# Kernel tuning notes

Measured on AMD Instinct MI355X. Metric: run time of the kernel, lower is better.

The kernel has to match this reference:

```python
import jax, jax.numpy as jnp
import numpy as np

# dims
B, QL, KL = 2, 1024, 4096
HID = 2048            # hidden_size
H, HD, RD = 16, 128, 64   # heads, head_dim, rope_dim
G = 4                 # gla_num_groups
HPG = H // G          # heads_per_group
QLR = 512             # q low-rank (W_dQ out)
LAT = 256             # latent_dim_per_group
KVP = G * LAT         # kv_proj_dim
EPS = 1e-6


def rmsnorm(x, w):
    var = jnp.mean(jnp.square(x.astype(jnp.float32)), axis=-1, keepdims=True)
    return (x * jax.lax.rsqrt(var + EPS)).astype(x.dtype) * w


def setup_inputs() -> dict:
    key = jax.random.key(0)
    ks = jax.random.split(key, 8)
    s = 0.02
    return {
        "x_q": jax.random.normal(ks[0], (B, QL, HID), jnp.float32),
        "x_kv": jax.random.normal(ks[1], (B, KL, HID), jnp.float32),
        "W_dQ": jax.random.normal(ks[2], (HID, QLR), jnp.float32) * s,
        "q_norm_w": jnp.ones((QLR,), jnp.float32),
        "W_uQ": jax.random.normal(ks[3], (QLR, H * (HD + RD)), jnp.float32) * s,
        "W_dKV": jax.random.normal(ks[4], (HID, KVP + RD), jnp.float32) * s,
        "kv_norm_w": jnp.ones((G, LAT), jnp.float32),
        "W_ukv": jax.random.normal(ks[5], (G, LAT, HPG * 2 * HD), jnp.float32) * s,
        "W_o": jax.random.normal(ks[6], (H * HD, HID), jnp.float32) * s,
    }


def reference(x_q, x_kv, W_dQ, q_norm_w, W_uQ, W_dKV, kv_norm_w, W_ukv, W_o):
    b, ql, _ = x_q.shape
    kl = x_kv.shape[1]
    # --- query path: down-proj -> RMSNorm -> up-proj -> drop rope dims ---
    q = rmsnorm(x_q @ W_dQ, q_norm_w)                       # [b, ql, QLR]
    q = (q @ W_uQ).reshape(b, ql, H, HD + RD)[..., :HD]     # [b, ql, H, HD]
    # --- kv path: down-proj -> slice -> per-group RMSNorm -> grouped up-proj ---
    ckv = (x_kv @ W_dKV)[..., :KVP].reshape(b, kl, G, LAT)  # [b, kl, G, LAT]
    ckv = rmsnorm(ckv, kv_norm_w)                           # weight [G, LAT] broadcasts
    kv = jnp.einsum("bsgl,gld->bsgd", ckv, W_ukv)           # [b, kl, G, HPG*2*HD]
    kv = kv.reshape(b, kl, H, 2 * HD)                       # group-major head order
    k, v = kv[..., :HD], kv[..., HD:]
    # --- SDPA (no mask, non-causal) ---
    scale = 1.0 / np.sqrt(HD).astype(np.float32)
    scores = jnp.einsum("bqhd,bkhd->bhqk", q, k) * scale    # [b, H, ql, kl]
    p = jax.nn.softmax(scores, axis=-1)
    out = jnp.einsum("bhqk,bkhd->bqhd", p, v).reshape(b, ql, H * HD)
    return out @ W_o
```

## Files before the change

kernel.cpp:

```cpp
#include <hip/hip_runtime.h>
#include <hip/hip_bf16.h>
#include <math.h>


typedef __attribute__((ext_vector_type(8))) short short8;
typedef __attribute__((ext_vector_type(4))) float f32x4;

__device__ __forceinline__ ushort f2bf(float x) {
    __hip_bfloat16 h = __float2bfloat16(x);
    return *reinterpret_cast<ushort*>(&h);
}

__global__ __launch_bounds__(256) void cast_bf16(const float* __restrict__ src,
        ushort* __restrict__ dst)
{
    size_t i = ((size_t)blockIdx.x * 256 + threadIdx.x) * 8;
    float4 a = *(const float4*)(src + i);
    float4 b = *(const float4*)(src + i + 4);
    ushort u[8] = {f2bf(a.x), f2bf(a.y), f2bf(a.z), f2bf(a.w),
                   f2bf(b.x), f2bf(b.y), f2bf(b.z), f2bf(b.w)};
    *(uint4*)(dst + i) = *(uint4*)u;
}

__global__ __launch_bounds__(256) void transpose_cast(const float* __restrict__ src,
        ushort* __restrict__ dst, int srl, int dstld, int remap,
        long src_z, long dst_z)
{
    __shared__ ushort tile[64][68];
    const int k0 = blockIdx.x * 64;
    const int n0 = blockIdx.y * 64;
    src += (size_t)blockIdx.z * src_z;
    dst += (size_t)blockIdx.z * dst_z;
    const int cb = n0 + (remap ? (n0 >> 7) * 64 : 0);
    const int t = threadIdx.x;
    {
        int r = t >> 4, c4 = t & 15;
        #pragma unroll
        for (int i = 0; i < 4; ++i) {
            float4 v = *(const float4*)(src + (size_t)(k0 + r + 16 * i) * srl + cb + c4 * 4);
            tile[r + 16 * i][c4 * 4 + 0] = f2bf(v.x);
            tile[r + 16 * i][c4 * 4 + 1] = f2bf(v.y);
            tile[r + 16 * i][c4 * 4 + 2] = f2bf(v.z);
            tile[r + 16 * i][c4 * 4 + 3] = f2bf(v.w);
        }
    }
    __syncthreads();
    {
        int n = t >> 4, k4 = t & 15;
        #pragma unroll
        for (int i = 0; i < 4; ++i) {
            ushort4 v;
            v.x = tile[k4 * 4 + 0][n + 16 * i];
            v.y = tile[k4 * 4 + 1][n + 16 * i];
            v.z = tile[k4 * 4 + 2][n + 16 * i];
            v.w = tile[k4 * 4 + 3][n + 16 * i];
            *(ushort4*)(dst + (size_t)(n0 + n + 16 * i) * dstld + k0 + k4 * 4) = v;
        }
    }
}

__global__ __launch_bounds__(256) void gemm_mfma(const ushort* __restrict__ A,
        const ushort* __restrict__ Bt, void* __restrict__ Cv,
        int M, int N, int K, int lda, int ldb, int ldc, int obf16, float scale)
{
    __shared__ ushort As[128][72];
    __shared__ ushort Bs[128][72];
    const int tid = threadIdx.x;
    const int w = tid >> 6, lane = tid & 63;
    const int quad = lane >> 4, l16 = lane & 15;
    const int wm = (w >> 1) * 64, wn = (w & 1) * 64;
    const int m0 = blockIdx.y * 128, n0 = blockIdx.x * 128;

    f32x4 acc[4][4];
    #pragma unroll
    for (int i = 0; i < 4; ++i)
        #pragma unroll
        for (int j = 0; j < 4; ++j) acc[i][j] = (f32x4){0.f, 0.f, 0.f, 0.f};

    const int str = tid >> 3;
    const int stc = (tid & 7) * 8;

    for (int k0 = 0; k0 < K; k0 += 64) {
        __syncthreads();
        #pragma unroll
        for (int i = 0; i < 4; ++i) {
            int r = str + 32 * i;
            *(uint4*)&As[r][stc] = *(const uint4*)(A + (size_t)(m0 + r) * lda + k0 + stc);
            *(uint4*)&Bs[r][stc] = *(const uint4*)(Bt + (size_t)(n0 + r) * ldb + k0 + stc);
        }
        __syncthreads();
        #pragma unroll
        for (int kc = 0; kc < 2; ++kc) {
            short8 af[4], bf[4];
            #pragma unroll
            for (int i = 0; i < 4; ++i) {
                af[i] = *(const short8*)&As[wm + i * 16 + l16][kc * 32 + quad * 8];
                bf[i] = *(const short8*)&Bs[wn + i * 16 + l16][kc * 32 + quad * 8];
            }
            #pragma unroll
            for (int i = 0; i < 4; ++i)
                #pragma unroll
                for (int j = 0; j < 4; ++j)
                    acc[i][j] = __builtin_amdgcn_mfma_f32_16x16x32_bf16(af[i], bf[j], acc[i][j], 0, 0, 0);
        }
    }
    if (!obf16) {
        float* C = (float*)Cv;
        #pragma unroll
        for (int i = 0; i < 4; ++i)
            #pragma unroll
            for (int r = 0; r < 4; ++r) {
                float* cp = C + (size_t)(m0 + wm + i * 16 + quad * 4 + r) * ldc + n0 + wn + l16;
                #pragma unroll
                for (int j = 0; j < 4; ++j) cp[j * 16] = acc[i][j][r] * scale;
            }
    } else {
        ushort* C = (ushort*)Cv;
        #pragma unroll
        for (int i = 0; i < 4; ++i)
            #pragma unroll
            for (int r = 0; r < 4; ++r) {
                ushort* cp = C + (size_t)(m0 + wm + i * 16 + quad * 4 + r) * ldc + n0 + wn + l16;
                #pragma unroll
                for (int j = 0; j < 4; ++j) cp[j * 16] = f2bf(acc[i][j][r] * scale);
            }
    }
}

__global__ __launch_bounds__(256) void rms_q_wave(const float* __restrict__ x,
        const float* __restrict__ w, ushort* __restrict__ dst)
{
    const int row = blockIdx.x * 4 + (threadIdx.x >> 6);
    const int lane = threadIdx.x & 63;
    const float* p = x + (size_t)row * 512;
    float4 v0 = *(const float4*)(p + lane * 4);
    float4 v1 = *(const float4*)(p + 256 + lane * 4);
    float ss = v0.x*v0.x + v0.y*v0.y + v0.z*v0.z + v0.w*v0.w
             + v1.x*v1.x + v1.y*v1.y + v1.z*v1.z + v1.w*v1.w;
    #pragma unroll
    for (int m = 1; m < 64; m <<= 1) ss += __shfl_xor(ss, m);
    float inv = rsqrtf(ss * (1.f / 512.f) + 1e-6f);
    float4 w0 = *(const float4*)(w + lane * 4);
    float4 w1 = *(const float4*)(w + 256 + lane * 4);
    ushort* dp = dst + (size_t)row * 512;
    ushort4 o0, o1;
    o0.x = f2bf(v0.x * inv * w0.x); o0.y = f2bf(v0.y * inv * w0.y);
    o0.z = f2bf(v0.z * inv * w0.z); o0.w = f2bf(v0.w * inv * w0.w);
    o1.x = f2bf(v1.x * inv * w1.x); o1.y = f2bf(v1.y * inv * w1.y);
    o1.z = f2bf(v1.z * inv * w1.z); o1.w = f2bf(v1.w * inv * w1.w);
    *(ushort4*)(dp + lane * 4)       = o0;
    *(ushort4*)(dp + 256 + lane * 4) = o1;
}

__global__ __launch_bounds__(256) void rms_kv_wave(const float* __restrict__ x,
        const float* __restrict__ w, ushort* __restrict__ dst)
{
    const int idx = blockIdx.x * 4 + (threadIdx.x >> 6);
    const int lane = threadIdx.x & 63;
    const int r = idx >> 2, g = idx & 3;
    const float* p = x + (size_t)r * 1024 + g * 256;
    float4 v = *(const float4*)(p + lane * 4);
    float ss = v.x*v.x + v.y*v.y + v.z*v.z + v.w*v.w;
    #pragma unroll
    for (int m = 1; m < 64; m <<= 1) ss += __shfl_xor(ss, m);
    float inv = rsqrtf(ss * (1.f / 256.f) + 1e-6f);
    float4 wv = *(const float4*)(w + g * 256 + lane * 4);
    ushort4 o;
    o.x = f2bf(v.x * inv * wv.x); o.y = f2bf(v.y * inv * wv.y);
    o.z = f2bf(v.z * inv * wv.z); o.w = f2bf(v.w * inv * wv.w);
    *(ushort4*)(dst + (size_t)r * 1024 + g * 256 + lane * 4) = o;
}

__global__ __launch_bounds__(256) void transpose_v(const ushort* __restrict__ KVb,
                                                   ushort* __restrict__ Vt)
{
    __shared__ ushort tile[64][66];
    const int s0 = blockIdx.x * 64;
    const int d0 = blockIdx.y * 64;
    const int bh = blockIdx.z;
    const int b = bh >> 4, h = bh & 15, g = h >> 2, p = h & 3;
    const int t = threadIdx.x;
    const ushort* src = KVb + (size_t)g * 8388608ull + (size_t)(b * 4096) * 1024 + p * 256 + 128;
    {
        int sl = t >> 4, c4 = t & 15;
        #pragma unroll
        for (int i = 0; i < 4; ++i) {
            int s = sl + 16 * i;
            ushort4 v = *(const ushort4*)(src + (size_t)(s0 + s) * 1024 + d0 + c4 * 4);
            tile[s][c4 * 4 + 0] = v.x; tile[s][c4 * 4 + 1] = v.y;
            tile[s][c4 * 4 + 2] = v.z; tile[s][c4 * 4 + 3] = v.w;
        }
    }
    __syncthreads();
    {
        int dl = t >> 4, s4 = t & 15;
        ushort* dst = Vt + (size_t)(b * 16 + h) * 128 * 4096;
        #pragma unroll
        for (int i = 0; i < 4; ++i) {
            int d = dl + 16 * i;
            ushort4 v;
            v.x = tile[s4 * 4 + 0][d]; v.y = tile[s4 * 4 + 1][d];
            v.z = tile[s4 * 4 + 2][d]; v.w = tile[s4 * 4 + 3][d];
            *(ushort4*)(dst + (size_t)(d0 + d) * 4096 + s0 + s4 * 4) = v;
        }
    }
}

__global__ __launch_bounds__(256) void attn_mfma_split(const ushort* __restrict__ Qb,
        const ushort* __restrict__ KVb, const ushort* __restrict__ Vt,
        float* __restrict__ Opart, float* __restrict__ ml)
{
    __shared__ ushort Ks[64][136];
    __shared__ ushort VsT[128][72];
    __shared__ ushort Ps[4][16][72];

    const int q0 = blockIdx.x * 64;
    const int h = blockIdx.y;
    const int b = blockIdx.z >> 1, chunk = blockIdx.z & 1;
    const int g = h >> 2, p = h & 3;
    const int tid = threadIdx.x;
    const int w = tid >> 6, lane = tid & 63;
    const int quad = lane >> 4, l16 = lane & 15;
    const int sbase = chunk * 2048;

    const ushort* qg = Qb + (size_t)(b * 1024 + q0) * 2048 + h * 128;
    const ushort* kg = KVb + (size_t)g * 8388608ull + (size_t)(b * 4096 + sbase) * 1024 + p * 256;
    const ushort* vg = Vt + (size_t)(b * 16 + h) * 128 * 4096 + sbase;

    {
        int r = tid >> 4, c8 = tid & 15;
        #pragma unroll
        for (int i = 0; i < 4; ++i)
            *(uint4*)&Ks[r + 16 * i][c8 * 8] =
                *(const uint4*)(qg + (size_t)(r + 16 * i) * 2048 + c8 * 8);
    }
    __syncthreads();
    short8 qf[4];
    {
        int qr = w * 16 + l16;
        #pragma unroll
        for (int kc = 0; kc < 4; ++kc)
            qf[kc] = *(const short8*)&Ks[qr][kc * 32 + quad * 8];
    }

    f32x4 accO[8];
    float m_i[4], l_i[4];
    #pragma unroll
    for (int dt = 0; dt < 8; ++dt) accO[dt] = (f32x4){0.f, 0.f, 0.f, 0.f};
    #pragma unroll
    for (int r = 0; r < 4; ++r) { m_i[r] = -INFINITY; l_i[r] = 0.f; }

    for (int s0 = 0; s0 < 2048; s0 += 64) {
        __syncthreads();
        {
            int r = tid >> 4, c8 = tid & 15;
            #pragma unroll
            for (int i = 0; i < 4; ++i)
                *(uint4*)&Ks[r + 16 * i][c8 * 8] =
                    *(const uint4*)(kg + (size_t)(s0 + r + 16 * i) * 1024 + c8 * 8);
            int d = tid >> 3, s8 = tid & 7;
            #pragma unroll
            for (int i = 0; i < 4; ++i)
                *(uint4*)&VsT[d + 32 * i][s8 * 8] =
                    *(const uint4*)(vg + (size_t)(d + 32 * i) * 4096 + s0 + s8 * 8);
        }
        __syncthreads();
        f32x4 accS[4];
        #pragma unroll
        for (int st = 0; st < 4; ++st) accS[st] = (f32x4){0.f, 0.f, 0.f, 0.f};
        #pragma unroll
        for (int kc = 0; kc < 4; ++kc) {
            #pragma unroll
            for (int st = 0; st < 4; ++st) {
                short8 kf = *(const short8*)&Ks[st * 16 + l16][kc * 32 + quad * 8];
                accS[st] = __builtin_amdgcn_mfma_f32_16x16x32_bf16(qf[kc], kf, accS[st], 0, 0, 0);
            }
        }
        #pragma unroll
        for (int r = 0; r < 4; ++r) {
            float tm = fmaxf(fmaxf(accS[0][r], accS[1][r]), fmaxf(accS[2][r], accS[3][r]));
            #pragma unroll
            for (int msk = 1; msk < 16; msk <<= 1) tm = fmaxf(tm, __shfl_xor(tm, msk));
            float mn = fmaxf(m_i[r], tm);
            float alpha = __expf(m_i[r] - mn);
            float rs = 0.f;
            #pragma unroll
            for (int st = 0; st < 4; ++st) {
                float e = __expf(accS[st][r] - mn);
                rs += e;
                Ps[w][quad * 4 + r][st * 16 + l16] = f2bf(e);
            }
            #pragma unroll
            for (int msk = 1; msk < 16; msk <<= 1) rs += __shfl_xor(rs, msk);
            l_i[r] = l_i[r] * alpha + rs;
            m_i[r] = mn;
            #pragma unroll
            for (int dt = 0; dt < 8; ++dt) accO[dt][r] *= alpha;
        }
        __syncthreads();
        short8 pf[2];
        #pragma unroll
        for (int sc = 0; sc < 2; ++sc)
            pf[sc] = *(const short8*)&Ps[w][l16][sc * 32 + quad * 8];
        #pragma unroll
        for (int sc = 0; sc < 2; ++sc) {
            #pragma unroll
            for (int dt = 0; dt < 8; ++dt) {
                short8 vf = *(const short8*)&VsT[dt * 16 + l16][sc * 32 + quad * 8];
                accO[dt] = __builtin_amdgcn_mfma_f32_16x16x32_bf16(pf[sc], vf, accO[dt], 0, 0, 0);
            }
        }
    }
    const int qrow = q0 + w * 16 + quad * 4;
    float* ob = Opart + (size_t)((chunk * 2 + b) * 1024 + qrow) * 2048 + h * 128 + l16;
    #pragma unroll
    for (int r = 0; r < 4; ++r)
        #pragma unroll
        for (int dt = 0; dt < 8; ++dt)
            ob[(size_t)r * 2048 + dt * 16] = accO[dt][r];
    if (l16 == 0) {
        #pragma unroll
        for (int r = 0; r < 4; ++r) {
            size_t mi = ((size_t)((chunk * 2 + b) * 1024 + qrow + r) * 16 + h) * 2;
            ml[mi] = m_i[r];
            ml[mi + 1] = l_i[r];
        }
    }
}

__global__ __launch_bounds__(256) void attn_merge(const float* __restrict__ Opart,
        const float* __restrict__ ml, ushort* __restrict__ Om)
{
    const int idx = blockIdx.x * 4 + (threadIdx.x >> 6);
    const int lane = threadIdx.x & 63;
    const int h = idx & 15;
    const int q = (idx >> 4) & 1023;
    const int b = idx >> 14;

    size_t m1i = ((size_t)((0 * 2 + b) * 1024 + q) * 16 + h) * 2;
    size_t m2i = ((size_t)((1 * 2 + b) * 1024 + q) * 16 + h) * 2;
    float m1 = ml[m1i], l1 = ml[m1i + 1];
    float m2 = ml[m2i], l2 = ml[m2i + 1];
    float M = fmaxf(m1, m2);
    float w1 = __expf(m1 - M), w2 = __expf(m2 - M);
    float invL = 1.f / (l1 * w1 + l2 * w2);

    const float* o1 = Opart + (size_t)((0 * 2 + b) * 1024 + q) * 2048 + h * 128;
    const float* o2 = Opart + (size_t)((1 * 2 + b) * 1024 + q) * 2048 + h * 128;
    ushort* ob = Om + (size_t)(b * 1024 + q) * 2048 + h * 128;
    ob[lane]      = f2bf((o1[lane]      * w1 + o2[lane]      * w2) * invL);
    ob[lane + 64] = f2bf((o1[lane + 64] * w1 + o2[lane + 64] * w2) * invL);
}

extern "C" void kernel_launch(void* const* d_in, const int* in_sizes, int n_in,
                              void* d_out, int out_size, void* d_ws, size_t ws_size,
                              hipStream_t stream)
{
    (void)in_sizes; (void)n_in; (void)out_size; (void)ws_size;
    const float* x_q       = (const float*)d_in[0];
    const float* x_kv      = (const float*)d_in[1];
    const float* W_dQ      = (const float*)d_in[2];
    const float* q_norm_w  = (const float*)d_in[3];
    const float* W_uQ      = (const float*)d_in[4];
    const float* W_dKV     = (const float*)d_in[5];
    const float* kv_norm_w = (const float*)d_in[6];
    const float* W_ukv     = (const float*)d_in[7];
    const float* W_o       = (const float*)d_in[8];
    float* out = (float*)d_out;

    float* ws = (float*)d_ws;
    ushort* xkvb       = (ushort*)ws;
    ushort* attn_out_b = (ushort*)ws;
    float*  mlbuf      = ws + 2097152ull;
    ushort* Wot        = (ushort*)(ws + 4194304ull);
    float*  ckv        = ws + 8388608ull;
    float*  Opart      = ws + 8388608ull;
    ushort* xqb        = (ushort*)(ws + 8388608ull);
    ushort* WdQt       = (ushort*)(ws + 10485760ull);
    float*  q_lat      = ws + 11010048ull;
    ushort* q_lat_b    = (ushort*)(ws + 12058624ull);
    ushort* WuQt       = (ushort*)(ws + 12582912ull);
    ushort* ckv_b      = (ushort*)(ws + 16777216ull);
    ushort* kvgb       = (ushort*)(ws + 20971520ull);
    ushort* vt         = (ushort*)(ws + 37748736ull);
    ushort* qb         = (ushort*)(ws + 46137344ull);
    ushort* WdKVt      = (ushort*)(ws + 48234496ull);
    ushort* Wukvt      = (ushort*)(ws + 49283072ull);

    const float qscale = 0.08838834764831845f;

    cast_bf16<<<2048, 256, 0, stream>>>(x_q, xqb);
    transpose_cast<<<dim3(32, 8, 1), 256, 0, stream>>>(W_dQ, WdQt, 512, 2048, 0, 0, 0);
    gemm_mfma<<<dim3(4, 16), 256, 0, stream>>>(xqb, WdQt, q_lat, 2048, 512, 2048, 2048, 2048, 512, 0, 1.f);
    rms_q_wave<<<512, 256, 0, stream>>>(q_lat, q_norm_w, q_lat_b);
    transpose_cast<<<dim3(8, 32, 1), 256, 0, stream>>>(W_uQ, WuQt, 3072, 512, 1, 0, 0);
    gemm_mfma<<<dim3(16, 16), 256, 0, stream>>>(q_lat_b, WuQt, qb, 2048, 2048, 512, 512, 512, 2048, 1, qscale);
    cast_bf16<<<8192, 256, 0, stream>>>(x_kv, xkvb);
    transpose_cast<<<dim3(32, 16, 1), 256, 0, stream>>>(W_dKV, WdKVt, 1088, 2048, 0, 0, 0);
    gemm_mfma<<<dim3(8, 64), 256, 0, stream>>>(xkvb, WdKVt, ckv, 8192, 1024, 2048, 2048, 2048, 1024, 0, 1.f);
    rms_kv_wave<<<8192, 256, 0, stream>>>(ckv, kv_norm_w, ckv_b);
    transpose_cast<<<dim3(4, 16, 4), 256, 0, stream>>>(W_ukv, Wukvt, 1024, 256, 0, 262144, 262144);
    for (int g = 0; g < 4; ++g)
        gemm_mfma<<<dim3(8, 64), 256, 0, stream>>>(ckv_b + g * 256, Wukvt + (size_t)g * 262144,
                                                   kvgb + (size_t)g * 8388608ull,
                                                   8192, 1024, 256, 1024, 256, 1024, 1, 1.f);
    transpose_v<<<dim3(64, 2, 32), 256, 0, stream>>>(kvgb, vt);
    attn_mfma_split<<<dim3(16, 16, 4), 256, 0, stream>>>(qb, kvgb, vt, Opart, mlbuf);
    attn_merge<<<8192, 256, 0, stream>>>(Opart, mlbuf, attn_out_b);
    transpose_cast<<<dim3(32, 32, 1), 256, 0, stream>>>(W_o, Wot, 2048, 2048, 0, 0, 0);
    gemm_mfma<<<dim3(16, 16), 256, 0, stream>>>(attn_out_b, Wot, out, 2048, 2048, 2048, 2048, 2048, 2048, 0, 1.f);
}
```

Before: 555.5 us.

## Double per-wave query rows in attention and batch grouped KV up-projection GEMMs

The attention kernel now handles 128 query rows per block, 32 per wave as two 16-row tiles, so each K and V tile loaded into shared memory feeds twice as many MFMAs. Query fragments now come straight from global memory instead of being staged through shared memory. The four per-group KV up-projection GEMM launches become one launch using blockIdx.z with batch strides. In exchange the attention grid is halved to 512 blocks and register pressure grows from the doubled accumulators, which may reduce occupancy.

Measured after the change: 580.7 us. +4.5%, slower.

```diff
diff --git a/kernel.cpp b/kernel.cpp
--- a/kernel.cpp
+++ b/kernel.cpp
@@ -61,7 +61,8 @@
 
 __global__ __launch_bounds__(256) void gemm_mfma(const ushort* __restrict__ A,
         const ushort* __restrict__ Bt, void* __restrict__ Cv,
-        int M, int N, int K, int lda, int ldb, int ldc, int obf16, float scale)
+        int M, int N, int K, int lda, int ldb, int ldc, int obf16, float scale,
+        long strA, long strB, long strC)
 {
     __shared__ ushort As[128][72];
     __shared__ ushort Bs[128][72];
@@ -70,6 +71,8 @@
     const int quad = lane >> 4, l16 = lane & 15;
     const int wm = (w >> 1) * 64, wn = (w & 1) * 64;
     const int m0 = blockIdx.y * 128, n0 = blockIdx.x * 128;
+    A  += (size_t)blockIdx.z * strA;
+    Bt += (size_t)blockIdx.z * strB;
 
     f32x4 acc[4][4];
     #pragma unroll
@@ -105,7 +108,7 @@
         }
     }
     if (!obf16) {
-        float* C = (float*)Cv;
+        float* C = (float*)Cv + (size_t)blockIdx.z * strC;
         #pragma unroll
         for (int i = 0; i < 4; ++i)
             #pragma unroll
@@ -115,7 +118,7 @@
                 for (int j = 0; j < 4; ++j) cp[j * 16] = acc[i][j][r] * scale;
             }
     } else {
-        ushort* C = (ushort*)Cv;
+        ushort* C = (ushort*)Cv + (size_t)blockIdx.z * strC;
         #pragma unroll
         for (int i = 0; i < 4; ++i)
             #pragma unroll
@@ -212,9 +215,9 @@
 {
     __shared__ ushort Ks[64][136];
     __shared__ ushort VsT[128][72];
-    __shared__ ushort Ps[4][16][72];
-
-    const int q0 = blockIdx.x * 64;
+    __shared__ ushort Ps[4][32][72];
+
+    const int q0 = blockIdx.x * 128;
     const int h = blockIdx.y;
     const int b = blockIdx.z >> 1, chunk = blockIdx.z & 1;
     const int g = h >> 2, p = h & 3;
@@ -227,28 +230,23 @@
     const ushort* kg = KVb + (size_t)g * 8388608ull + (size_t)(b * 4096 + sbase) * 1024 + p * 256;
     const ushort* vg = Vt + (size_t)(b * 16 + h) * 128 * 4096 + sbase;
 
-    {
-        int r = tid >> 4, c8 = tid & 15;
-        #pragma unroll
-        for (int i = 0; i < 4; ++i)
-            *(uint4*)&Ks[r + 16 * i][c8 * 8] =
-                *(const uint4*)(qg + (size_t)(r + 16 * i) * 2048 + c8 * 8);
-    }
-    __syncthreads();
-    short8 qf[4];
-    {
-        int qr = w * 16 + l16;
+    short8 qf[2][4];
+    #pragma unroll
+    for (int qt = 0; qt < 2; ++qt)
         #pragma unroll
         for (int kc = 0; kc < 4; ++kc)
-            qf[kc] = *(const short8*)&Ks[qr][kc * 32 + quad * 8];
-    }
-
-    f32x4 accO[8];
-    float m_i[4], l_i[4];
-    #pragma unroll
-    for (int dt = 0; dt < 8; ++dt) accO[dt] = (f32x4){0.f, 0.f, 0.f, 0.f};
-    #pragma unroll
-    for (int r = 0; r < 4; ++r) { m_i[r] = -INFINITY; l_i[r] = 0.f; }
+            qf[qt][kc] = *(const short8*)(qg + (size_t)(w * 32 + qt * 16 + l16) * 2048
+                                          + kc * 32 + quad * 8);
+
+    f32x4 accO[2][8];
+    float m_i[2][4], l_i[2][4];
+    #pragma unroll
+    for (int qt = 0; qt < 2; ++qt) {
+        #pragma unroll
+        for (int dt = 0; dt < 8; ++dt) accO[qt][dt] = (f32x4){0.f, 0.f, 0.f, 0.f};
+        #pragma unroll
+        for (int r = 0; r < 4; ++r) { m_i[qt][r] = -INFINITY; l_i[qt][r] = 0.f; }
+    }
 
     for (int s0 = 0; s0 < 2048; s0 += 64) {
         __syncthreads();
@@ -265,65 +263,79 @@
                     *(const uint4*)(vg + (size_t)(d + 32 * i) * 4096 + s0 + s8 * 8);
         }
         __syncthreads();
-        f32x4 accS[4];
-        #pragma unroll
-        for (int st = 0; st < 4; ++st) accS[st] = (f32x4){0.f, 0.f, 0.f, 0.f};
+        f32x4 accS[2][4];
+        #pragma unroll
+        for (int qt = 0; qt < 2; ++qt)
+            #pragma unroll
+            for (int st = 0; st < 4; ++st) accS[qt][st] = (f32x4){0.f, 0.f, 0.f, 0.f};
         #pragma unroll
         for (int kc = 0; kc < 4; ++kc) {
-            #pragma unroll
-            for (int st = 0; st < 4; ++st) {
-                short8 kf = *(const short8*)&Ks[st * 16 + l16][kc * 32 + quad * 8];
-                accS[st] = __builtin_amdgcn_mfma_f32_16x16x32_bf16(qf[kc], kf, accS[st], 0, 0, 0);
-            }
-        }
-        #pragma unroll
-        for (int r = 0; r < 4; ++r) {
-            float tm = fmaxf(fmaxf(accS[0][r], accS[1][r]), fmaxf(accS[2][r], accS[3][r]));
-            #pragma unroll
-            for (int msk = 1; msk < 16; msk <<= 1) tm = fmaxf(tm, __shfl_xor(tm, msk));
-            float mn = fmaxf(m_i[r], tm);
-            float alpha = __expf(m_i[r] - mn);
-            float rs = 0.f;
-            #pragma unroll
-            for (int st = 0; st < 4; ++st) {
-                float e = __expf(accS[st][r] - mn);
-                rs += e;
-                Ps[w][quad * 4 + r][st * 16 + l16] = f2bf(e);
-            }
-            #pragma unroll
-            for (int msk = 1; msk < 16; msk <<= 1) rs += __shfl_xor(rs, msk);
-            l_i[r] = l_i[r] * alpha + rs;
-            m_i[r] = mn;
-            #pragma unroll
-            for (int dt = 0; dt < 8; ++dt) accO[dt][r] *= alpha;
-        }
+            short8 kf[4];
+            #pragma unroll
+            for (int st = 0; st < 4; ++st)
+                kf[st] = *(const short8*)&Ks[st * 16 + l16][kc * 32 + quad * 8];
+            #pragma unroll
+            for (int qt = 0; qt < 2; ++qt)
+                #pragma unroll
+                for (int st = 0; st < 4; ++st)
+                    accS[qt][st] = __builtin_amdgcn_mfma_f32_16x16x32_bf16(qf[qt][kc], kf[st], accS[qt][st], 0, 0, 0);
+        }
+        #pragma unroll
+        for (int qt = 0; qt < 2; ++qt)
+            #pragma unroll
+            for (int r = 0; r < 4; ++r) {
+                float tm = fmaxf(fmaxf(accS[qt][0][r], accS[qt][1][r]),
+                                 fmaxf(accS[qt][2][r], accS[qt][3][r]));
+                #pragma unroll
+                for (int msk = 1; msk < 16; msk <<= 1) tm = fmaxf(tm, __shfl_xor(tm, msk));
+                float mn = fmaxf(m_i[qt][r], tm);
+                float alpha = __expf(m_i[qt][r] - mn);
+                float rs = 0.f;
+                #pragma unroll
+                for (int st = 0; st < 4; ++st) {
+                    float e = __expf(accS[qt][st][r] - mn);
+                    rs += e;
+                    Ps[w][qt * 16 + quad * 4 + r][st * 16 + l16] = f2bf(e);
+                }
+                #pragma unroll
+                for (int msk = 1; msk < 16; msk <<= 1) rs += __shfl_xor(rs, msk);
+                l_i[qt][r] = l_i[qt][r] * alpha + rs;
+                m_i[qt][r] = mn;
+                #pragma unroll
+                for (int dt = 0; dt < 8; ++dt) accO[qt][dt][r] *= alpha;
+            }
         __syncthreads();
-        short8 pf[2];
-        #pragma unroll
-        for (int sc = 0; sc < 2; ++sc)
-            pf[sc] = *(const short8*)&Ps[w][l16][sc * 32 + quad * 8];
         #pragma unroll
         for (int sc = 0; sc < 2; ++sc) {
+            short8 pf[2];
+            #pragma unroll
+            for (int qt = 0; qt < 2; ++qt)
+                pf[qt] = *(const short8*)&Ps[w][qt * 16 + l16][sc * 32 + quad * 8];
             #pragma unroll
             for (int dt = 0; dt < 8; ++dt) {
                 short8 vf = *(const short8*)&VsT[dt * 16 + l16][sc * 32 + quad * 8];
-                accO[dt] = __builtin_amdgcn_mfma_f32_16x16x32_bf16(pf[sc], vf, accO[dt], 0, 0, 0);
-            }
-        }
-    }
-    const int qrow = q0 + w * 16 + quad * 4;
-    float* ob = Opart + (size_t)((chunk * 2 + b) * 1024 + qrow) * 2048 + h * 128 + l16;
-    #pragma unroll
-    for (int r = 0; r < 4; ++r)
-        #pragma unroll
-        for (int dt = 0; dt < 8; ++dt)
-            ob[(size_t)r * 2048 + dt * 16] = accO[dt][r];
-    if (l16 == 0) {
-        #pragma unroll
-        for (int r = 0; r < 4; ++r) {
-            size_t mi = ((size_t)((chunk * 2 + b) * 1024 + qrow + r) * 16 + h) * 2;
-            ml[mi] = m_i[r];
-            ml[mi + 1] = l_i[r];
+                #pragma unroll
+                for (int qt = 0; qt < 2; ++qt)
+                    accO[qt][dt] = __builtin_amdgcn_mfma_f32_16x16x32_bf16(pf[qt], vf, accO[qt][dt], 0, 0, 0);
+            }
+        }
+    }
+    #pragma unroll
+    for (int qt = 0; qt < 2; ++qt) {
+        const int qrow = q0 + w * 32 + qt * 16 + quad * 4;
+        float* ob = Opart + (size_t)((chunk * 2 + b) * 1024 + qrow) * 2048 + h * 128 + l16;
+        #pragma unroll
+        for (int r = 0; r < 4; ++r)
+            #pragma unroll
+            for (int dt = 0; dt < 8; ++dt)
+                ob[(size_t)r * 2048 + dt * 16] = accO[qt][dt][r];
+        if (l16 == 0) {
+            #pragma unroll
+            for (int r = 0; r < 4; ++r) {
+                size_t mi = ((size_t)((chunk * 2 + b) * 1024 + qrow + r) * 16 + h) * 2;
+                ml[mi] = m_i[qt][r];
+                ml[mi + 1] = l_i[qt][r];
+            }
         }
     }
 }
@@ -391,22 +403,21 @@
 
     cast_bf16<<<2048, 256, 0, stream>>>(x_q, xqb);
     transpose_cast<<<dim3(32, 8, 1), 256, 0, stream>>>(W_dQ, WdQt, 512, 2048, 0, 0, 0);
-    gemm_mfma<<<dim3(4, 16), 256, 0, stream>>>(xqb, WdQt, q_lat, 2048, 512, 2048, 2048, 2048, 512, 0, 1.f);
+    gemm_mfma<<<dim3(4, 16), 256, 0, stream>>>(xqb, WdQt, q_lat, 2048, 512, 2048, 2048, 2048, 512, 0, 1.f, 0, 0, 0);
     rms_q_wave<<<512, 256, 0, stream>>>(q_lat, q_norm_w, q_lat_b);
     transpose_cast<<<dim3(8, 32, 1), 256, 0, stream>>>(W_uQ, WuQt, 3072, 512, 1, 0, 0);
-    gemm_mfma<<<dim3(16, 16), 256, 0, stream>>>(q_lat_b, WuQt, qb, 2048, 2048, 512, 512, 512, 2048, 1, qscale);
+    gemm_mfma<<<dim3(16, 16), 256, 0, stream>>>(q_lat_b, WuQt, qb, 2048, 2048, 512, 512, 512, 2048, 1, qscale, 0, 0, 0);
     cast_bf16<<<8192, 256, 0, stream>>>(x_kv, xkvb);
     transpose_cast<<<dim3(32, 16, 1), 256, 0, stream>>>(W_dKV, WdKVt, 1088, 2048, 0, 0, 0);
-    gemm_mfma<<<dim3(8, 64), 256, 0, stream>>>(xkvb, WdKVt, ckv, 8192, 1024, 2048, 2048, 2048, 1024, 0, 1.f);
+    gemm_mfma<<<dim3(8, 64), 256, 0, stream>>>(xkvb, WdKVt, ckv, 8192, 1024, 2048, 2048, 2048, 1024, 0, 1.f, 0, 0, 0);
     rms_kv_wave<<<8192, 256, 0, stream>>>(ckv, kv_norm_w, ckv_b);
     transpose_cast<<<dim3(4, 16, 4), 256, 0, stream>>>(W_ukv, Wukvt, 1024, 256, 0, 262144, 262144);
-    for (int g = 0; g < 4; ++g)
-        gemm_mfma<<<dim3(8, 64), 256, 0, stream>>>(ckv_b + g * 256, Wukvt + (size_t)g * 262144,
-                                                   kvgb + (size_t)g * 8388608ull,
-                                                   8192, 1024, 256, 1024, 256, 1024, 1, 1.f);
+    gemm_mfma<<<dim3(8, 64, 4), 256, 0, stream>>>(ckv_b, Wukvt, kvgb,
+                                                  8192, 1024, 256, 1024, 256, 1024, 1, 1.f,
+                                                  256, 262144, 8388608);
     transpose_v<<<dim3(64, 2, 32), 256, 0, stream>>>(kvgb, vt);
-    attn_mfma_split<<<dim3(16, 16, 4), 256, 0, stream>>>(qb, kvgb, vt, Opart, mlbuf);
+    attn_mfma_split<<<dim3(8, 16, 4), 256, 0, stream>>>(qb, kvgb, vt, Opart, mlbuf);
     attn_merge<<<8192, 256, 0, stream>>>(Opart, mlbuf, attn_out_b);
     transpose_cast<<<dim3(32, 32, 1), 256, 0, stream>>>(W_o, Wot, 2048, 2048, 0, 0, 0);
-    gemm_mfma<<<dim3(16, 16), 256, 0, stream>>>(attn_out_b, Wot, out, 2048, 2048, 2048, 2048, 2048, 2048, 0, 1.f);
-}
+    gemm_mfma<<<dim3(16, 16), 256, 0, stream>>>(attn_out_b, Wot, out, 2048, 2048, 2048, 2048, 2048, 2048, 0, 1.f, 0, 0, 0);
+}
```

## Use direct global-to-LDS loads in GEMM and batch grouped up-projection

Applied to the files above, without the earlier changes.

The GEMM staging now uses the global_load_lds builtin to copy A and B tiles straight into shared memory, skipping register round-trips. The shared tiles lose their row padding so they match the direct-load layout. The four per-group KV up-projection GEMMs become one launch with a z-dimension and strides. The unpadded LDS layout may add bank conflicts on the MFMA fragment reads.

New measurement: 567.9 us. +2.2%, slower.

```diff
diff --git a/kernel.cpp b/kernel.cpp
--- a/kernel.cpp
+++ b/kernel.cpp
@@ -9,6 +9,12 @@
 __device__ __forceinline__ ushort f2bf(float x) {
     __hip_bfloat16 h = __float2bfloat16(x);
     return *reinterpret_cast<ushort*>(&h);
+}
+
+__device__ __forceinline__ void gl2lds16(const ushort* g, ushort* l) {
+    __builtin_amdgcn_global_load_lds(
+        (const __attribute__((address_space(1))) unsigned int*)g,
+        (__attribute__((address_space(3))) unsigned int*)l, 16, 0, 0);
 }
 
 __global__ __launch_bounds__(256) void cast_bf16(const float* __restrict__ src,
@@ -61,15 +67,18 @@
 
 __global__ __launch_bounds__(256) void gemm_mfma(const ushort* __restrict__ A,
         const ushort* __restrict__ Bt, void* __restrict__ Cv,
-        int M, int N, int K, int lda, int ldb, int ldc, int obf16, float scale)
-{
-    __shared__ ushort As[128][72];
-    __shared__ ushort Bs[128][72];
+        int M, int N, int K, int lda, int ldb, int ldc, int obf16, float scale,
+        long strA, long strB, long strC)
+{
+    __shared__ ushort As[128 * 64];
+    __shared__ ushort Bs[128 * 64];
     const int tid = threadIdx.x;
     const int w = tid >> 6, lane = tid & 63;
     const int quad = lane >> 4, l16 = lane & 15;
     const int wm = (w >> 1) * 64, wn = (w & 1) * 64;
     const int m0 = blockIdx.y * 128, n0 = blockIdx.x * 128;
+    A  += (size_t)blockIdx.z * strA;
+    Bt += (size_t)blockIdx.z * strB;
 
     f32x4 acc[4][4];
     #pragma unroll
@@ -77,16 +86,16 @@
         #pragma unroll
         for (int j = 0; j < 4; ++j) acc[i][j] = (f32x4){0.f, 0.f, 0.f, 0.f};
 
-    const int str = tid >> 3;
-    const int stc = (tid & 7) * 8;
+    const int lr = lane >> 3;
+    const int lc = (lane & 7) * 8;
 
     for (int k0 = 0; k0 < K; k0 += 64) {
         __syncthreads();
         #pragma unroll
         for (int i = 0; i < 4; ++i) {
-            int r = str + 32 * i;
-            *(uint4*)&As[r][stc] = *(const uint4*)(A + (size_t)(m0 + r) * lda + k0 + stc);
-            *(uint4*)&Bs[r][stc] = *(const uint4*)(Bt + (size_t)(n0 + r) * ldb + k0 + stc);
+            int r0 = w * 32 + i * 8;
+            gl2lds16(A  + (size_t)(m0 + r0 + lr) * lda + k0 + lc, &As[r0 * 64]);
+            gl2lds16(Bt + (size_t)(n0 + r0 + lr) * ldb + k0 + lc, &Bs[r0 * 64]);
         }
         __syncthreads();
         #pragma unroll
@@ -94,8 +103,8 @@
             short8 af[4], bf[4];
             #pragma unroll
             for (int i = 0; i < 4; ++i) {
-                af[i] = *(const short8*)&As[wm + i * 16 + l16][kc * 32 + quad * 8];
-                bf[i] = *(const short8*)&Bs[wn + i * 16 + l16][kc * 32 + quad * 8];
+                af[i] = *(const short8*)&As[(wm + i * 16 + l16) * 64 + kc * 32 + quad * 8];
+                bf[i] = *(const short8*)&Bs[(wn + i * 16 + l16) * 64 + kc * 32 + quad * 8];
             }
             #pragma unroll
             for (int i = 0; i < 4; ++i)
@@ -105,7 +114,7 @@
         }
     }
     if (!obf16) {
-        float* C = (float*)Cv;
+        float* C = (float*)Cv + (size_t)blockIdx.z * strC;
         #pragma unroll
         for (int i = 0; i < 4; ++i)
             #pragma unroll
@@ -115,7 +124,7 @@
                 for (int j = 0; j < 4; ++j) cp[j * 16] = acc[i][j][r] * scale;
             }
     } else {
-        ushort* C = (ushort*)Cv;
+        ushort* C = (ushort*)Cv + (size_t)blockIdx.z * strC;
         #pragma unroll
         for (int i = 0; i < 4; ++i)
             #pragma unroll
@@ -391,22 +400,21 @@
 
     cast_bf16<<<2048, 256, 0, stream>>>(x_q, xqb);
     transpose_cast<<<dim3(32, 8, 1), 256, 0, stream>>>(W_dQ, WdQt, 512, 2048, 0, 0, 0);
-    gemm_mfma<<<dim3(4, 16), 256, 0, stream>>>(xqb, WdQt, q_lat, 2048, 512, 2048, 2048, 2048, 512, 0, 1.f);
+    gemm_mfma<<<dim3(4, 16), 256, 0, stream>>>(xqb, WdQt, q_lat, 2048, 512, 2048, 2048, 2048, 512, 0, 1.f, 0, 0, 0);
     rms_q_wave<<<512, 256, 0, stream>>>(q_lat, q_norm_w, q_lat_b);
     transpose_cast<<<dim3(8, 32, 1), 256, 0, stream>>>(W_uQ, WuQt, 3072, 512, 1, 0, 0);
-    gemm_mfma<<<dim3(16, 16), 256, 0, stream>>>(q_lat_b, WuQt, qb, 2048, 2048, 512, 512, 512, 2048, 1, qscale);
+    gemm_mfma<<<dim3(16, 16), 256, 0, stream>>>(q_lat_b, WuQt, qb, 2048, 2048, 512, 512, 512, 2048, 1, qscale, 0, 0, 0);
     cast_bf16<<<8192, 256, 0, stream>>>(x_kv, xkvb);
     transpose_cast<<<dim3(32, 16, 1), 256, 0, stream>>>(W_dKV, WdKVt, 1088, 2048, 0, 0, 0);
-    gemm_mfma<<<dim3(8, 64), 256, 0, stream>>>(xkvb, WdKVt, ckv, 8192, 1024, 2048, 2048, 2048, 1024, 0, 1.f);
+    gemm_mfma<<<dim3(8, 64), 256, 0, stream>>>(xkvb, WdKVt, ckv, 8192, 1024, 2048, 2048, 2048, 1024, 0, 1.f, 0, 0, 0);
     rms_kv_wave<<<8192, 256, 0, stream>>>(ckv, kv_norm_w, ckv_b);
     transpose_cast<<<dim3(4, 16, 4), 256, 0, stream>>>(W_ukv, Wukvt, 1024, 256, 0, 262144, 262144);
-    for (int g = 0; g < 4; ++g)
-        gemm_mfma<<<dim3(8, 64), 256, 0, stream>>>(ckv_b + g * 256, Wukvt + (size_t)g * 262144,
-                                                   kvgb + (size_t)g * 8388608ull,
-                                                   8192, 1024, 256, 1024, 256, 1024, 1, 1.f);
+    gemm_mfma<<<dim3(8, 64, 4), 256, 0, stream>>>(ckv_b, Wukvt, kvgb,
+                                                  8192, 1024, 256, 1024, 256, 1024, 1, 1.f,
+                                                  256, 262144, 8388608);
     transpose_v<<<dim3(64, 2, 32), 256, 0, stream>>>(kvgb, vt);
     attn_mfma_split<<<dim3(16, 16, 4), 256, 0, stream>>>(qb, kvgb, vt, Opart, mlbuf);
     attn_merge<<<8192, 256, 0, stream>>>(Opart, mlbuf, attn_out_b);
     transpose_cast<<<dim3(32, 32, 1), 256, 0, stream>>>(W_o, Wot, 2048, 2048, 0, 0, 0);
-    gemm_mfma<<<dim3(16, 16), 256, 0, stream>>>(attn_out_b, Wot, out, 2048, 2048, 2048, 2048, 2048, 2048, 0, 1.f);
-}
+    gemm_mfma<<<dim3(16, 16), 256, 0, stream>>>(attn_out_b, Wot, out, 2048, 2048, 2048, 2048, 2048, 2048, 0, 1.f, 0, 0, 0);
+}
```
